# Optimization experiments

Hardware: AMD Instinct MI355X
Metric: run time of the kernel (lower is better)

## Reference

```python
import jax, jax.numpy as jnp
import numpy as np

N_NODES = 50000
N_EDGES = 800000


def _sage_conv(h, ei, W_l, W_r, b_l):
    """PyG SAGEConv: lin_l(mean_{j->i} h_j) + lin_r(h_i). lin_l has bias, lin_r does not."""
    src, dst = ei[0], ei[1]
    # mean-aggregate raw features first (linear commutes with mean) to avoid [E, out] intermediates
    msum = jax.ops.segment_sum(h[src], dst, num_segments=N_NODES)          # [N, d]
    cnt = jax.ops.segment_sum(jnp.ones((ei.shape[1], 1), h.dtype), dst,
                              num_segments=N_NODES)                         # [N, 1]
    mean = msum / jnp.maximum(cnt, 1.0)
    return mean @ W_l + b_l + h @ W_r


def setup_inputs() -> dict:
    key = jax.random.key(0)
    ks = jax.random.split(key, 8)
    d_in, d_hid, d_out = 64, 64, 32
    return {
        "x": jax.random.normal(ks[0], (N_NODES, d_in), dtype=jnp.float32),
        "ei0": jax.random.randint(ks[1], (2, N_EDGES), 0, N_NODES, dtype=jnp.int32),
        "ei1": jax.random.randint(ks[2], (2, N_EDGES), 0, N_NODES, dtype=jnp.int32),
        "Wl": jax.random.normal(ks[3], (2, 2, d_in, d_hid), dtype=jnp.float32) * 0.05,
        "Wr": jax.random.normal(ks[4], (2, 2, d_in, d_hid), dtype=jnp.float32) * 0.05,
        "bl": jax.random.normal(ks[5], (2, 2, d_hid), dtype=jnp.float32) * 0.05,
        "lin_W": jax.random.normal(ks[6], (d_hid, d_out), dtype=jnp.float32) * 0.05,
        "lin_b": jax.random.normal(ks[7], (d_out,), dtype=jnp.float32) * 0.05,
    }


def reference(x, ei0, ei1, Wl, Wr, bl, lin_W, lin_b):
    edge_indices = (ei0, ei1)  # one edge_index per relation
    h = x
    for l in range(2):  # layers (structurally fixed)
        out = None
        for r, ei in enumerate(edge_indices):  # HeteroConv aggr='sum' over relations
            y = _sage_conv(h, ei, Wl[l, r], Wr[l, r], bl[l, r])
            out = y if out is None else out + y
        h = jax.nn.relu(out)
    return h @ lin_W + lin_b
```

## Files before the change

kernel.cpp:

```cpp
#include <hip/hip_runtime.h>

#define NN 50000
#define CAP 32
#define OVF_CAP 4096
#define SHARD_W 12500
#define NCH 64

__device__ __forceinline__ unsigned short f2bf(float f) {
    unsigned u = __float_as_uint(f);
    u += 0x7fffu + ((u >> 16) & 1u);
    return (unsigned short)(u >> 16);
}
__device__ __forceinline__ float bf2f(unsigned short u) {
    return __uint_as_float(((unsigned)u) << 16);
}

__global__ __launch_bounds__(256) void init_fuse(
    const float* __restrict__ in, unsigned short* __restrict__ out, int n4,
    int* __restrict__ zbuf, int nint)
{
    int stride = gridDim.x * blockDim.x;
    int id0 = blockIdx.x * blockDim.x + threadIdx.x;
    for (int i = id0; i < n4; i += stride) {
        float4 v = ((const float4*)in)[i];
        ushort4 o;
        o.x = f2bf(v.x); o.y = f2bf(v.y); o.z = f2bf(v.z); o.w = f2bf(v.w);
        ((ushort4*)out)[i] = o;
    }
    for (int i = id0; i < nint; i += stride) zbuf[i] = 0;
}


__global__ __launch_bounds__(256) void count_pass(
    const int* __restrict__ ei0, int E0,
    const int* __restrict__ ei1, int E1,
    unsigned char* __restrict__ cnt)
{
    __shared__ int lcnt[SHARD_W];
    int q   = blockIdx.x & 3;
    int c   = (blockIdx.x >> 2) & (NCH - 1);
    int rel = blockIdx.x >> 8;
    const int* ei = rel ? ei1 : ei0;
    int E         = rel ? E1  : E0;
    int ce = (E + NCH - 1) / NCH;
    int lo = c * ce;
    int hi = min(lo + ce, E);
    int nlo = q * SHARD_W;

    for (int i = threadIdx.x; i < SHARD_W; i += 256) lcnt[i] = 0;
    __syncthreads();
    for (int t = lo + threadIdx.x; t < hi; t += 256) {
        int loc = ei[E + t] - nlo;
        if ((unsigned)loc < (unsigned)SHARD_W) atomicAdd(&lcnt[loc], 1);
    }
    __syncthreads();
    unsigned char* dst = cnt + ((size_t)(rel * NCH + c)) * NN + nlo;
    for (int i = threadIdx.x; i < SHARD_W / 4; i += 256) {
        uchar4 v;
        v.x = (unsigned char)min(lcnt[4 * i + 0], 255);
        v.y = (unsigned char)min(lcnt[4 * i + 1], 255);
        v.z = (unsigned char)min(lcnt[4 * i + 2], 255);
        v.w = (unsigned char)min(lcnt[4 * i + 3], 255);
        ((uchar4*)dst)[i] = v;
    }
}

__global__ __launch_bounds__(256) void prefix_pass(
    const unsigned char* __restrict__ cnt,
    unsigned char* __restrict__ bases,
    int* __restrict__ deg)
{
    int t = blockIdx.x * 256 + threadIdx.x;
    if (t >= 2 * (NN / 4)) return;
    int rel = t / (NN / 4);
    int n4  = (t % (NN / 4)) * 4;

    unsigned run0 = 0, run1 = 0, run2 = 0, run3 = 0;
    #pragma unroll
    for (int c = 0; c < NCH; c++) {
        size_t idx = ((size_t)(rel * NCH + c)) * NN + n4;
        unsigned v = *(const unsigned*)&cnt[idx];
        unsigned b0 = min(run0, 255u), b1 = min(run1, 255u);
        unsigned b2 = min(run2, 255u), b3 = min(run3, 255u);
        *(unsigned*)&bases[idx] = b0 | (b1 << 8) | (b2 << 16) | (b3 << 24);
        run0 += v & 255u;
        run1 += (v >> 8) & 255u;
        run2 += (v >> 16) & 255u;
        run3 += (v >> 24);
    }
    *(int4*)&deg[rel * NN + n4] = make_int4(run0, run1, run2, run3);
}

__global__ __launch_bounds__(256) void place_pass(
    const int* __restrict__ ei0, int E0,
    const int* __restrict__ ei1, int E1,
    const unsigned char* __restrict__ bases,
    unsigned short* __restrict__ bins,
    int2* __restrict__ ovf, int* __restrict__ ovf_cnt)
{
    __shared__ int lcnt[SHARD_W];
    __shared__ __align__(16) unsigned char lbase[SHARD_W];
    int q   = blockIdx.x & 3;
    int c   = (blockIdx.x >> 2) & (NCH - 1);
    int rel = blockIdx.x >> 8;
    const int* ei = rel ? ei1 : ei0;
    int E         = rel ? E1  : E0;
    int ce = (E + NCH - 1) / NCH;
    int lo = c * ce;
    int hi = min(lo + ce, E);
    int nlo = q * SHARD_W;

    const unsigned char* bsrc = bases + ((size_t)(rel * NCH + c)) * NN + nlo;
    for (int i = threadIdx.x; i < SHARD_W / 4; i += 256)
        ((unsigned*)lbase)[i] = ((const unsigned*)bsrc)[i];
    for (int i = threadIdx.x; i < SHARD_W; i += 256) lcnt[i] = 0;
    __syncthreads();

    int taskbase = rel * NN + nlo;
    for (int t = lo + threadIdx.x; t < hi; t += 256) {
        int loc = ei[E + t] - nlo;
        if ((unsigned)loc < (unsigned)SHARD_W) {
            int s = ei[t];
            int r = atomicAdd(&lcnt[loc], 1);
            int slot = (int)lbase[loc] + r;
            int task = taskbase + loc;
            if (slot < CAP) {
                bins[(size_t)task * CAP + slot] = (unsigned short)s;
            } else {
                int o = atomicAdd(ovf_cnt, 1);
                if (o < OVF_CAP) ovf[o] = make_int2(task, s);
            }
        }
    }
}

__global__ __launch_bounds__(256) void aggregate(
    const unsigned short* __restrict__ bins, const int* __restrict__ deg,
    const unsigned short* __restrict__ hb, unsigned short* __restrict__ agg,
    const int2* __restrict__ ovf, const int* __restrict__ ovf_cnt)
{
    int lane = threadIdx.x & 63;
    int half = lane >> 5;
    int p = lane & 31;
    int wid = (blockIdx.x * blockDim.x + threadIdx.x) >> 6;
    int nwaves = (gridDim.x * blockDim.x) >> 6;
    const unsigned int* hb32 = (const unsigned int*)hb;
    unsigned int* agg32 = (unsigned int*)agg;

    for (int task = wid; task < 2 * NN; task += nwaves) {
        int d = deg[task];
        int m = min(d, CAP);
        int idx = 0;
        if (lane < m) idx = bins[(size_t)task * CAP + lane];
        float a00=0.f,a01=0.f, a10=0.f,a11=0.f, a20=0.f,a21=0.f, a30=0.f,a31=0.f;
        int F = m >> 1;
        int q = 0;
        for (; q + 4 <= F; q += 4) {
            int s0 = __shfl(idx, 2*(q+0) + half);
            int s1 = __shfl(idx, 2*(q+1) + half);
            int s2 = __shfl(idx, 2*(q+2) + half);
            int s3 = __shfl(idx, 2*(q+3) + half);
            unsigned u0 = hb32[(size_t)s0 * 32 + p];
            unsigned u1 = hb32[(size_t)s1 * 32 + p];
            unsigned u2 = hb32[(size_t)s2 * 32 + p];
            unsigned u3 = hb32[(size_t)s3 * 32 + p];
            a00 += __uint_as_float(u0 << 16); a01 += __uint_as_float(u0 & 0xffff0000u);
            a10 += __uint_as_float(u1 << 16); a11 += __uint_as_float(u1 & 0xffff0000u);
            a20 += __uint_as_float(u2 << 16); a21 += __uint_as_float(u2 & 0xffff0000u);
            a30 += __uint_as_float(u3 << 16); a31 += __uint_as_float(u3 & 0xffff0000u);
        }
        for (; q < F; ++q) {
            int s = __shfl(idx, 2*q + half);
            unsigned u = hb32[(size_t)s * 32 + p];
            a00 += __uint_as_float(u << 16); a01 += __uint_as_float(u & 0xffff0000u);
        }
        if (m & 1) {
            int s = __shfl(idx, m - 1);
            if (half == 0) {
                unsigned u = hb32[(size_t)s * 32 + p];
                a00 += __uint_as_float(u << 16); a01 += __uint_as_float(u & 0xffff0000u);
            }
        }
        if (d > CAP) {
            int cnt = min(*ovf_cnt, OVF_CAP);
            for (int e = 0; e < cnt; ++e) {
                int2 v = ovf[e];
                if (v.x == task && half == 0) {
                    unsigned u = hb32[(size_t)v.y * 32 + p];
                    a00 += __uint_as_float(u << 16); a01 += __uint_as_float(u & 0xffff0000u);
                }
            }
        }
        float s0 = (a00 + a10) + (a20 + a30);
        float s1 = (a01 + a11) + (a21 + a31);
        s0 += __shfl_xor(s0, 32);
        s1 += __shfl_xor(s1, 32);
        if (half == 0) {
            float inv = 1.0f / (float)max(d, 1);
            unsigned lo = (unsigned)f2bf(s0 * inv);
            unsigned hi = (unsigned)f2bf(s1 * inv);
            agg32[(size_t)task * 32 + p] = lo | (hi << 16);
        }
    }
}

#define RST 132
__global__ __launch_bounds__(256) void layer_gemm(
    const unsigned short* __restrict__ agg0, const unsigned short* __restrict__ agg1,
    const unsigned short* __restrict__ selfb,
    const float* __restrict__ Wl0, const float* __restrict__ Wl1,
    const float* __restrict__ Wr0, const float* __restrict__ Wr1,
    const float* __restrict__ b0, const float* __restrict__ b1,
    unsigned short* __restrict__ hb16)
{
    __shared__ float Wch[64 * 64];
    __shared__ float rowsT[64 * RST];
    __shared__ float bias[64];

    int tid = threadIdx.x;
    int base = blockIdx.x * 128;
    if (tid < 64) bias[tid] = b0[tid] + b1[tid];

    int j8 = (tid & 7) * 8;
    int n4 = (tid >> 3) * 4;

    float acc[4][8];
    #pragma unroll
    for (int i = 0; i < 4; i++)
        #pragma unroll
        for (int c = 0; c < 8; c++) acc[i][c] = 0.f;

    for (int chunk = 0; chunk < 3; chunk++) {
        const float* W = (chunk == 0) ? Wl0 : (chunk == 1) ? Wl1 : Wr0;
        const unsigned short* src = (chunk == 0) ? agg0 : (chunk == 1) ? agg1 : selfb;
        __syncthreads();
        #pragma unroll
        for (int r = 0; r < 4; r++) {
            int i = tid + 256 * r;
            float4 w = *(const float4*)&W[i * 4];
            if (chunk == 2) {
                float4 w2 = *(const float4*)&Wr1[i * 4];
                w.x += w2.x; w.y += w2.y; w.z += w2.z; w.w += w2.w;
            }
            *(float4*)&Wch[i * 4] = w;
        }
        #pragma unroll
        for (int r = 0; r < 8; r++) {
            int i = tid + 256 * r;
            int node = i >> 4;
            int k4 = (i & 15) * 4;
            int g = base + node;
            ushort4 u = make_ushort4(0, 0, 0, 0);
            if (g < NN) u = *(const ushort4*)&src[(size_t)g * 64 + k4];
            rowsT[(k4 + 0) * RST + node] = bf2f(u.x);
            rowsT[(k4 + 1) * RST + node] = bf2f(u.y);
            rowsT[(k4 + 2) * RST + node] = bf2f(u.z);
            rowsT[(k4 + 3) * RST + node] = bf2f(u.w);
        }
        __syncthreads();
        #pragma unroll 4
        for (int k = 0; k < 64; k++) {
            float4 wa = *(const float4*)&Wch[k * 64 + j8];
            float4 wb = *(const float4*)&Wch[k * 64 + j8 + 4];
            float4 rv = *(const float4*)&rowsT[k * RST + n4];
            float w[8] = {wa.x, wa.y, wa.z, wa.w, wb.x, wb.y, wb.z, wb.w};
            float rr[4] = {rv.x, rv.y, rv.z, rv.w};
            #pragma unroll
            for (int i = 0; i < 4; i++)
                #pragma unroll
                for (int c = 0; c < 8; c++)
                    acc[i][c] = fmaf(rr[i], w[c], acc[i][c]);
        }
    }

    #pragma unroll
    for (int i = 0; i < 4; i++) {
        int g = base + n4 + i;
        if (g < NN) {
            ushort4 p0, p1;
            p0.x = f2bf(fmaxf(acc[i][0] + bias[j8 + 0], 0.f));
            p0.y = f2bf(fmaxf(acc[i][1] + bias[j8 + 1], 0.f));
            p0.z = f2bf(fmaxf(acc[i][2] + bias[j8 + 2], 0.f));
            p0.w = f2bf(fmaxf(acc[i][3] + bias[j8 + 3], 0.f));
            p1.x = f2bf(fmaxf(acc[i][4] + bias[j8 + 4], 0.f));
            p1.y = f2bf(fmaxf(acc[i][5] + bias[j8 + 5], 0.f));
            p1.z = f2bf(fmaxf(acc[i][6] + bias[j8 + 6], 0.f));
            p1.w = f2bf(fmaxf(acc[i][7] + bias[j8 + 7], 0.f));
            *(ushort4*)&hb16[(size_t)g * 64 + j8]     = p0;
            *(ushort4*)&hb16[(size_t)g * 64 + j8 + 4] = p1;
        }
    }
}

__global__ __launch_bounds__(256) void layer_gemm_final(
    const unsigned short* __restrict__ agg0, const unsigned short* __restrict__ agg1,
    const unsigned short* __restrict__ selfb,
    const float* __restrict__ Wl0, const float* __restrict__ Wl1,
    const float* __restrict__ Wr0, const float* __restrict__ Wr1,
    const float* __restrict__ b0, const float* __restrict__ b1,
    const float* __restrict__ linW, const float* __restrict__ linb,
    float* __restrict__ out)
{
    __shared__ float Wch[64 * 64];
    __shared__ float rowsT[64 * RST];
    __shared__ float bias[64];

    int tid = threadIdx.x;
    int base = blockIdx.x * 128;
    if (tid < 64) bias[tid] = b0[tid] + b1[tid];

    int j8 = (tid & 7) * 8;
    int n4 = (tid >> 3) * 4;

    float acc[4][8];
    #pragma unroll
    for (int i = 0; i < 4; i++)
        #pragma unroll
        for (int c = 0; c < 8; c++) acc[i][c] = 0.f;

    for (int chunk = 0; chunk < 3; chunk++) {
        const float* W = (chunk == 0) ? Wl0 : (chunk == 1) ? Wl1 : Wr0;
        const unsigned short* src = (chunk == 0) ? agg0 : (chunk == 1) ? agg1 : selfb;
        __syncthreads();
        #pragma unroll
        for (int r = 0; r < 4; r++) {
            int i = tid + 256 * r;
            float4 w = *(const float4*)&W[i * 4];
            if (chunk == 2) {
                float4 w2 = *(const float4*)&Wr1[i * 4];
                w.x += w2.x; w.y += w2.y; w.z += w2.z; w.w += w2.w;
            }
            *(float4*)&Wch[i * 4] = w;
        }
        #pragma unroll
        for (int r = 0; r < 8; r++) {
            int i = tid + 256 * r;
            int node = i >> 4;
            int k4 = (i & 15) * 4;
            int g = base + node;
            ushort4 u = make_ushort4(0, 0, 0, 0);
            if (g < NN) u = *(const ushort4*)&src[(size_t)g * 64 + k4];
            rowsT[(k4 + 0) * RST + node] = bf2f(u.x);
            rowsT[(k4 + 1) * RST + node] = bf2f(u.y);
            rowsT[(k4 + 2) * RST + node] = bf2f(u.z);
            rowsT[(k4 + 3) * RST + node] = bf2f(u.w);
        }
        __syncthreads();
        #pragma unroll 4
        for (int k = 0; k < 64; k++) {
            float4 wa = *(const float4*)&Wch[k * 64 + j8];
            float4 wb = *(const float4*)&Wch[k * 64 + j8 + 4];
            float4 rv = *(const float4*)&rowsT[k * RST + n4];
            float w[8] = {wa.x, wa.y, wa.z, wa.w, wb.x, wb.y, wb.z, wb.w};
            float rr[4] = {rv.x, rv.y, rv.z, rv.w};
            #pragma unroll
            for (int i = 0; i < 4; i++)
                #pragma unroll
                for (int c = 0; c < 8; c++)
                    acc[i][c] = fmaf(rr[i], w[c], acc[i][c]);
        }
    }

    float o[4][8];
    #pragma unroll
    for (int i = 0; i < 4; i++)
        #pragma unroll
        for (int c = 0; c < 8; c++)
            o[i][c] = fmaxf(acc[i][c] + bias[j8 + c], 0.f);

    __syncthreads();

    #pragma unroll
    for (int r = 0; r < 2; r++) {
        int i = tid + 256 * r;
        *(float4*)&Wch[i * 4] = *(const float4*)&linW[i * 4];
    }
    if (tid < 32) bias[tid] = linb[tid];
    #pragma unroll
    for (int i = 0; i < 4; i++)
        #pragma unroll
        for (int c = 0; c < 8; c++)
            rowsT[(j8 + c) * RST + (n4 + i)] = o[i][c];
    __syncthreads();

    int j4 = (tid & 7) * 4;
    float acc2[4][4];
    #pragma unroll
    for (int i = 0; i < 4; i++)
        #pragma unroll
        for (int c = 0; c < 4; c++) acc2[i][c] = 0.f;
    #pragma unroll 4
    for (int k = 0; k < 64; k++) {
        float4 w = *(const float4*)&Wch[k * 32 + j4];
        float4 rv = *(const float4*)&rowsT[k * RST + n4];
        float wr[4] = {w.x, w.y, w.z, w.w};
        float rr[4] = {rv.x, rv.y, rv.z, rv.w};
        #pragma unroll
        for (int i = 0; i < 4; i++)
            #pragma unroll
            for (int c = 0; c < 4; c++)
                acc2[i][c] = fmaf(rr[i], wr[c], acc2[i][c]);
    }
    #pragma unroll
    for (int i = 0; i < 4; i++) {
        int g = base + n4 + i;
        if (g < NN) {
            float4 ov;
            ov.x = acc2[i][0] + bias[j4 + 0];
            ov.y = acc2[i][1] + bias[j4 + 1];
            ov.z = acc2[i][2] + bias[j4 + 2];
            ov.w = acc2[i][3] + bias[j4 + 3];
            *(float4*)&out[(size_t)g * 32 + j4] = ov;
        }
    }
}

extern "C" void kernel_launch(void* const* d_in, const int* in_sizes, int n_in,
                              void* d_out, int out_size, void* d_ws, size_t ws_size,
                              hipStream_t stream)
{
    const float* x    = (const float*)d_in[0];
    const int*   ei0  = (const int*)d_in[1];
    const int*   ei1  = (const int*)d_in[2];
    const float* Wl   = (const float*)d_in[3];
    const float* Wr   = (const float*)d_in[4];
    const float* bl   = (const float*)d_in[5];
    const float* linW = (const float*)d_in[6];
    const float* linb = (const float*)d_in[7];
    float* out = (float*)d_out;

    int E0 = in_sizes[1] / 2;
    int E1 = in_sizes[2] / 2;

    unsigned short* bins = (unsigned short*)d_ws;
    unsigned short* aggb = bins + (size_t)2 * NN * CAP;
    unsigned short* agg0 = aggb;
    unsigned short* agg1 = aggb + (size_t)NN * 64;
    unsigned short* xb   = aggb + (size_t)2 * NN * 64;
    unsigned short* h1b  = xb + (size_t)NN * 64;
    int*  deg     = (int*)(h1b + (size_t)NN * 64);
    int*  ovf_cnt = deg + 2 * NN;
    int2* ovf     = (int2*)(ovf_cnt + 8);
    unsigned char* cnt   = (unsigned char*)bins;
    unsigned char* bases = (unsigned char*)aggb;

    dim3 blk(256);
    int ggrid = (NN + 127) / 128;

    init_fuse<<<1024, blk, 0, stream>>>(x, xb, NN * 16, ovf_cnt, 8);

    count_pass<<<2 * NCH * 4, blk, 0, stream>>>(ei0, E0, ei1, E1, cnt);
    prefix_pass<<<(2 * (NN / 4) + 255) / 256, blk, 0, stream>>>(cnt, bases, deg);
    place_pass<<<2 * NCH * 4, blk, 0, stream>>>(ei0, E0, ei1, E1, bases,
                                                bins, ovf, ovf_cnt);

    aggregate<<<4096, blk, 0, stream>>>(bins, deg, xb, aggb, ovf, ovf_cnt);
    layer_gemm<<<ggrid, blk, 0, stream>>>(agg0, agg1, xb,
        Wl + 0, Wl + 4096, Wr + 0, Wr + 4096, bl + 0, bl + 64, h1b);

    aggregate<<<4096, blk, 0, stream>>>(bins, deg, h1b, aggb, ovf, ovf_cnt);
    layer_gemm_final<<<ggrid, blk, 0, stream>>>(agg0, agg1, h1b,
        Wl + 8192, Wl + 12288, Wr + 8192, Wr + 12288, bl + 128, bl + 192,
        linW, linb, out);
}
```

Before: 278.3 us.

## Halve node shards and pack LDS counters into 16-bit halves for occupancy

The count and place passes now split the node range into 8 shards instead of 4, and store per-node counters as packed 16-bit pairs in 32-bit LDS words. This shrinks shared memory per block from about 50-62 KB to about 12-18 KB, so more blocks can be resident per CU, and doubles the grid to 1024 blocks. In exchange, each block now scans its whole edge chunk while keeping only half as many edges, so global edge-index reads double, and packed atomics add contention between neighbouring node pairs.

```diff
diff --git a/kernel.cpp b/kernel.cpp
--- a/kernel.cpp
+++ b/kernel.cpp
@@ -3,7 +3,8 @@
 #define NN 50000
 #define CAP 32
 #define OVF_CAP 4096
-#define SHARD_W 12500
+#define SHARD_W 6250
+#define NSH 8
 #define NCH 64
 
 __device__ __forceinline__ unsigned short f2bf(float f) {
@@ -31,15 +32,15 @@
 }
 
 
-__global__ __launch_bounds__(256) void count_pass(
+__global__ __launch_bounds__(256, 6) void count_pass(
     const int* __restrict__ ei0, int E0,
     const int* __restrict__ ei1, int E1,
     unsigned char* __restrict__ cnt)
 {
-    __shared__ int lcnt[SHARD_W];
-    int q   = blockIdx.x & 3;
-    int c   = (blockIdx.x >> 2) & (NCH - 1);
-    int rel = blockIdx.x >> 8;
+    __shared__ unsigned int lcnt32[SHARD_W / 2];
+    int q   = blockIdx.x & (NSH - 1);
+    int c   = (blockIdx.x >> 3) & (NCH - 1);
+    int rel = blockIdx.x >> 9;
     const int* ei = rel ? ei1 : ei0;
     int E         = rel ? E1  : E0;
     int ce = (E + NCH - 1) / NCH;
@@ -47,21 +48,21 @@
     int hi = min(lo + ce, E);
     int nlo = q * SHARD_W;
 
-    for (int i = threadIdx.x; i < SHARD_W; i += 256) lcnt[i] = 0;
+    for (int i = threadIdx.x; i < SHARD_W / 2; i += 256) lcnt32[i] = 0;
     __syncthreads();
     for (int t = lo + threadIdx.x; t < hi; t += 256) {
         int loc = ei[E + t] - nlo;
-        if ((unsigned)loc < (unsigned)SHARD_W) atomicAdd(&lcnt[loc], 1);
+        if ((unsigned)loc < (unsigned)SHARD_W)
+            atomicAdd(&lcnt32[loc >> 1], 1u << ((loc & 1) << 4));
     }
     __syncthreads();
-    unsigned char* dst = cnt + ((size_t)(rel * NCH + c)) * NN + nlo;
-    for (int i = threadIdx.x; i < SHARD_W / 4; i += 256) {
-        uchar4 v;
-        v.x = (unsigned char)min(lcnt[4 * i + 0], 255);
-        v.y = (unsigned char)min(lcnt[4 * i + 1], 255);
-        v.z = (unsigned char)min(lcnt[4 * i + 2], 255);
-        v.w = (unsigned char)min(lcnt[4 * i + 3], 255);
-        ((uchar4*)dst)[i] = v;
+    unsigned short* dst =
+        (unsigned short*)(cnt + ((size_t)(rel * NCH + c)) * NN + nlo);
+    for (int i = threadIdx.x; i < SHARD_W / 2; i += 256) {
+        unsigned w = lcnt32[i];
+        unsigned a = min(w & 0xffffu, 255u);
+        unsigned b = min(w >> 16, 255u);
+        dst[i] = (unsigned short)(a | (b << 8));
     }
 }
 
@@ -91,18 +92,18 @@
     *(int4*)&deg[rel * NN + n4] = make_int4(run0, run1, run2, run3);
 }
 
-__global__ __launch_bounds__(256) void place_pass(
+__global__ __launch_bounds__(256, 6) void place_pass(
     const int* __restrict__ ei0, int E0,
     const int* __restrict__ ei1, int E1,
     const unsigned char* __restrict__ bases,
     unsigned short* __restrict__ bins,
     int2* __restrict__ ovf, int* __restrict__ ovf_cnt)
 {
-    __shared__ int lcnt[SHARD_W];
-    __shared__ __align__(16) unsigned char lbase[SHARD_W];
-    int q   = blockIdx.x & 3;
-    int c   = (blockIdx.x >> 2) & (NCH - 1);
-    int rel = blockIdx.x >> 8;
+    __shared__ unsigned int lcnt32[SHARD_W / 2];
+    __shared__ unsigned short lbase16[SHARD_W / 2];
+    int q   = blockIdx.x & (NSH - 1);
+    int c   = (blockIdx.x >> 3) & (NCH - 1);
+    int rel = blockIdx.x >> 9;
     const int* ei = rel ? ei1 : ei0;
     int E         = rel ? E1  : E0;
     int ce = (E + NCH - 1) / NCH;
@@ -110,10 +111,12 @@
     int hi = min(lo + ce, E);
     int nlo = q * SHARD_W;
 
-    const unsigned char* bsrc = bases + ((size_t)(rel * NCH + c)) * NN + nlo;
-    for (int i = threadIdx.x; i < SHARD_W / 4; i += 256)
-        ((unsigned*)lbase)[i] = ((const unsigned*)bsrc)[i];
-    for (int i = threadIdx.x; i < SHARD_W; i += 256) lcnt[i] = 0;
+    const unsigned short* bsrc =
+        (const unsigned short*)(bases + ((size_t)(rel * NCH + c)) * NN + nlo);
+    for (int i = threadIdx.x; i < SHARD_W / 2; i += 256) {
+        lbase16[i] = bsrc[i];
+        lcnt32[i] = 0;
+    }
     __syncthreads();
 
     int taskbase = rel * NN + nlo;
@@ -121,8 +124,11 @@
         int loc = ei[E + t] - nlo;
         if ((unsigned)loc < (unsigned)SHARD_W) {
             int s = ei[t];
-            int r = atomicAdd(&lcnt[loc], 1);
-            int slot = (int)lbase[loc] + r;
+            int sh = (loc & 1) << 4;
+            unsigned r32 = atomicAdd(&lcnt32[loc >> 1], 1u << sh);
+            int r = (int)((r32 >> sh) & 0xffffu);
+            int b = (int)((lbase16[loc >> 1] >> ((loc & 1) << 3)) & 0xffu);
+            int slot = b + r;
             int task = taskbase + loc;
             if (slot < CAP) {
                 bins[(size_t)task * CAP + slot] = (unsigned short)s;
@@ -449,10 +455,10 @@
 
     init_fuse<<<1024, blk, 0, stream>>>(x, xb, NN * 16, ovf_cnt, 8);
 
-    count_pass<<<2 * NCH * 4, blk, 0, stream>>>(ei0, E0, ei1, E1, cnt);
+    count_pass<<<2 * NCH * NSH, blk, 0, stream>>>(ei0, E0, ei1, E1, cnt);
     prefix_pass<<<(2 * (NN / 4) + 255) / 256, blk, 0, stream>>>(cnt, bases, deg);
-    place_pass<<<2 * NCH * 4, blk, 0, stream>>>(ei0, E0, ei1, E1, bases,
-                                                bins, ovf, ovf_cnt);
+    place_pass<<<2 * NCH * NSH, blk, 0, stream>>>(ei0, E0, ei1, E1, bases,
+                                                  bins, ovf, ovf_cnt);
 
     aggregate<<<4096, blk, 0, stream>>>(bins, deg, xb, aggb, ovf, ovf_cnt);
     layer_gemm<<<ggrid, blk, 0, stream>>>(agg0, agg1, xb,
```

Result: faster. 272.6 us (-2.1%).
